# Optimization experiments

Measured on AMD Instinct MI355X. Metric: run time of the kernel, lower is better.

Reference implementation:

```python
import jax, jax.numpy as jnp
import numpy as np

N = 100000      # nodes
E = 1600000     # edges (avg degree 16)
IN = 512        # input feature dim
H, C = 8, 8     # conv1: 8 heads x 8 channels (hardcoded in module)
HID = H * C     # 64
OUT = 64        # output classes (conv2: 1 head, no concat)
NEG_SLOPE = 0.2 # PyG GATConv default leaky-relu slope


def setup_inputs() -> dict:
    key = jax.random.key(0)
    ks = jax.random.split(key, 10)
    x = jax.random.normal(ks[0], (N, IN), dtype=jnp.float32)
    edge_index = jax.random.randint(ks[1], (2, E), 0, N, dtype=jnp.int32)
    W1 = jax.random.normal(ks[2], (IN, HID), dtype=jnp.float32) / np.sqrt(IN).astype(np.float32)
    a_src1 = jax.random.normal(ks[3], (H, C), dtype=jnp.float32) * 0.1
    a_dst1 = jax.random.normal(ks[4], (H, C), dtype=jnp.float32) * 0.1
    b1 = jnp.zeros((HID,), dtype=jnp.float32)
    W2 = jax.random.normal(ks[5], (HID, OUT), dtype=jnp.float32) / np.sqrt(HID).astype(np.float32)
    a_src2 = jax.random.normal(ks[6], (1, OUT), dtype=jnp.float32) * 0.1
    a_dst2 = jax.random.normal(ks[7], (1, OUT), dtype=jnp.float32) * 0.1
    b2 = jnp.zeros((OUT,), dtype=jnp.float32)
    return {"x": x, "edge_index": edge_index, "W1": W1, "a_src1": a_src1,
            "a_dst1": a_dst1, "b1": b1, "W2": W2, "a_src2": a_src2,
            "a_dst2": a_dst2, "b2": b2}


def _gat_attend(h, src, dst, a_s, a_d, n_nodes):
    """h: [N,H,C]; src/dst: [E]; a_s/a_d: [H,C] -> aggregated [N,H,C]."""
    # per-node half-scores (PyG decomposition of a^T [Wx_i || Wx_j])
    sc_s = jnp.sum(h * a_s, axis=-1)                       # [N,H]
    sc_d = jnp.sum(h * a_d, axis=-1)                       # [N,H]
    logits = jax.nn.leaky_relu(sc_s[src] + sc_d[dst], NEG_SLOPE)  # [E,H]
    # segment softmax over edges grouped by destination node
    mx = jax.ops.segment_max(logits, dst, num_segments=n_nodes)   # [N,H]
    ex = jnp.exp(logits - mx[dst])                          # [E,H]
    denom = jax.ops.segment_sum(ex, dst, num_segments=n_nodes)    # [N,H]
    alpha = ex / (denom[dst] + 1e-16)                       # [E,H]
    msg = h[src] * alpha[:, :, None]                        # [E,H,C]
    return jax.ops.segment_sum(msg, dst, num_segments=n_nodes)    # [N,H,C]


def reference(x, edge_index, W1, a_src1, a_dst1, b1, W2, a_src2, a_dst2, b2):
    n = x.shape[0]
    loop = jnp.arange(n, dtype=edge_index.dtype)
    src = jnp.concatenate([edge_index[0], loop])            # self-loops (PyG default)
    dst = jnp.concatenate([edge_index[1], loop])
    # conv1: 8 heads, concat
    h1 = (x @ W1).reshape(n, H, C)
    o1 = _gat_attend(h1, src, dst, a_src1, a_dst1, n).reshape(n, HID) + b1
    x2 = jax.nn.elu(o1)
    # conv2: 1 head, no concat
    h2 = (x2 @ W2).reshape(n, 1, OUT)
    o2 = _gat_attend(h2, src, dst, a_src2, a_dst2, n)[:, 0] + b2
    return jax.nn.log_softmax(o2, axis=1)
```

## Files before the change

### kernel.cpp

```cpp
#include <hip/hip_runtime.h>
#include <cstdint>
#include <cstddef>

#define LEAKY 0.2f
#define NEG_INF -3.402823466e38f
static const int CHUNK = 2048;

typedef __attribute__((ext_vector_type(8))) short short8;
typedef __attribute__((ext_vector_type(4))) float floatx4;

__device__ __forceinline__ unsigned short f2bf(float f) {
    unsigned u = __float_as_uint(f);
    u += 0x7fffu + ((u >> 16) & 1u);
    return (unsigned short)(u >> 16);
}
__device__ __forceinline__ float bf2f(unsigned short u) {
    return __uint_as_float(((unsigned)u) << 16);
}
__device__ __forceinline__ float bflo(unsigned u) { return __uint_as_float(u << 16); }
__device__ __forceinline__ float bfhi(unsigned u) { return __uint_as_float(u & 0xffff0000u); }

__global__ __launch_bounds__(256) void k_misc(const float* __restrict__ W1, unsigned short* __restrict__ W1t,
                                              int* __restrict__ deg, int Nn) {
    int i = blockIdx.x * 256 + threadIdx.x;
    if (i < 64 * 512) {
        int n = i >> 9, k = i & 511;
        W1t[i] = f2bf(W1[k * 64 + n]);
    }
    if (i < Nn) deg[i] = 1;
}

__global__ __launch_bounds__(256) void k_mega1(const float* __restrict__ A, const unsigned short* __restrict__ W1t,
                                               unsigned short* __restrict__ C,
                                               const float* __restrict__ as1, const float* __restrict__ ad1,
                                               float* __restrict__ scs, float* __restrict__ scd, int M,
                                               const int* __restrict__ ei, int* __restrict__ deg, int E, int G1) {
    __shared__ __align__(16) unsigned short As[128][40];
    __shared__ __align__(16) unsigned short Bs[64][40];

    if ((int)blockIdx.x >= G1) {
        int cb = blockIdx.x - G1;
        int part = cb & 7;
        int Nn = M;
        int lo = (int)((long long)Nn * part >> 3);
        int hi = (int)((long long)Nn * (part + 1) >> 3);
        int nthr = (1024 >> 3) * 256;
        int tid = (cb >> 3) * 256 + threadIdx.x;
        for (int e = tid; e < E; e += nthr) {
            int d = ei[E + e];
            if (d >= lo && d < hi) atomicAdd(&deg[d], 1);
        }
        return;
    }

    int t = threadIdx.x;
    int w = t >> 6, l = t & 63;
    int quad = l >> 4, lm = l & 15;
    int row0 = blockIdx.x * 128;

    floatx4 acc[2][4] = {};

    for (int k0 = 0; k0 < 512; k0 += 32) {
#pragma unroll
        for (int j = 0; j < 4; ++j) {
            int f = t + 256 * j;
            int r = f >> 3, c4 = f & 7;
            int rg = row0 + r; if (rg >= M) rg = M - 1;
            float4 v = *(const float4*)(A + (size_t)rg * 512 + k0 + c4 * 4);
            ushort4 b; b.x = f2bf(v.x); b.y = f2bf(v.y); b.z = f2bf(v.z); b.w = f2bf(v.w);
            *(ushort4*)&As[r][c4 * 4] = b;
        }
        {
            int n = t >> 2, seg = t & 3;
            *(uint4*)&Bs[n][seg * 8] = *(const uint4*)(W1t + (size_t)n * 512 + k0 + seg * 8);
        }
        __syncthreads();

        short8 af[2], bfm[4];
#pragma unroll
        for (int tm = 0; tm < 2; ++tm) {
            int m = w * 32 + tm * 16 + lm;
            af[tm] = *(const short8*)&As[m][quad * 8];
        }
#pragma unroll
        for (int tn = 0; tn < 4; ++tn) {
            int n = tn * 16 + lm;
            bfm[tn] = *(const short8*)&Bs[n][quad * 8];
        }
#pragma unroll
        for (int tm = 0; tm < 2; ++tm)
#pragma unroll
            for (int tn = 0; tn < 4; ++tn)
                acc[tm][tn] = __builtin_amdgcn_mfma_f32_16x16x32_bf16(af[tm], bfm[tn], acc[tm][tn], 0, 0, 0);
        __syncthreads();
    }

    float as_l[4], ad_l[4];
#pragma unroll
    for (int tn = 0; tn < 4; ++tn) { as_l[tn] = as1[tn * 16 + lm]; ad_l[tn] = ad1[tn * 16 + lm]; }
    int hbase = (l >> 3) & 1;

#pragma unroll
    for (int tm = 0; tm < 2; ++tm) {
#pragma unroll
        for (int r = 0; r < 4; ++r) {
            int row = row0 + w * 32 + tm * 16 + quad * 4 + r;
            if (row < M) {
#pragma unroll
                for (int tn = 0; tn < 4; ++tn)
                    C[(size_t)row * 64 + tn * 16 + lm] = f2bf(acc[tm][tn][r]);
                float ps[4], pd[4];
#pragma unroll
                for (int tn = 0; tn < 4; ++tn) {
                    ps[tn] = acc[tm][tn][r] * as_l[tn];
                    pd[tn] = acc[tm][tn][r] * ad_l[tn];
                }
#pragma unroll
                for (int o = 1; o < 8; o <<= 1) {
#pragma unroll
                    for (int tn = 0; tn < 4; ++tn) {
                        ps[tn] += __shfl_xor(ps[tn], o);
                        pd[tn] += __shfl_xor(pd[tn], o);
                    }
                }
                if ((l & 7) == 0) {
#pragma unroll
                    for (int tn = 0; tn < 4; ++tn) {
                        scs[(size_t)row * 8 + tn * 2 + hbase] = ps[tn];
                        scd[(size_t)row * 8 + tn * 2 + hbase] = pd[tn];
                    }
                }
            }
        }
    }
}

__global__ __launch_bounds__(256) void k_scan1(const int* __restrict__ deg, int* __restrict__ bsum, int Nn) {
    __shared__ int sm[256];
    int b = blockIdx.x, t = threadIdx.x;
    int s = 0;
    int i0 = b * CHUNK + t * 8;
#pragma unroll
    for (int j = 0; j < 8; ++j) { int i = i0 + j; if (i < Nn) s += deg[i]; }
    sm[t] = s;
    __syncthreads();
    for (int o = 128; o; o >>= 1) { if (t < o) sm[t] += sm[t + o]; __syncthreads(); }
    if (t == 0) bsum[b] = sm[0];
}

__global__ __launch_bounds__(256) void k_scan3(const int* __restrict__ deg, const int* __restrict__ bsum,
                                               int* __restrict__ indptr, int* __restrict__ cursor,
                                               int Nn, int B) {
    __shared__ int wsum[4];
    int b = blockIdx.x, t = threadIdx.x, lane = t & 63, w = t >> 6;

    int vb = (lane < B) ? bsum[lane] : 0;
    int incb = vb;
#pragma unroll
    for (int o = 1; o < 64; o <<= 1) { int u = __shfl_up(incb, o); if (lane >= o) incb += u; }
    int bpre_b = __shfl(incb - vb, b);

    int i0 = b * CHUNK + t * 8;
    int d[8]; int s = 0;
#pragma unroll
    for (int j = 0; j < 8; ++j) { int i = i0 + j; d[j] = (i < Nn) ? deg[i] : 0; s += d[j]; }
    int inc = s;
#pragma unroll
    for (int o = 1; o < 64; o <<= 1) { int u = __shfl_up(inc, o); if (lane >= o) inc += u; }
    if (lane == 63) wsum[w] = inc;
    __syncthreads();
    int wofs = 0;
    for (int k = 0; k < w; ++k) wofs += wsum[k];
    int base = bpre_b + wofs + (inc - s);
    int run = 0;
#pragma unroll
    for (int j = 0; j < 8; ++j) {
        int i = i0 + j;
        if (i < Nn) {
            int v = base + run;
            indptr[i] = v; cursor[i] = v;
            run += d[j];
            if (i == Nn - 1) indptr[Nn] = v + d[j];
        }
    }
}

__global__ __launch_bounds__(256) void k_fill_p(const int* __restrict__ ei, int* __restrict__ cursor,
                                                int* __restrict__ csr, int E, int Nn) {
    int part = blockIdx.x & 7;
    int lo = (int)((long long)Nn * part >> 3);
    int hi = (int)((long long)Nn * (part + 1) >> 3);
    int nthr = (gridDim.x >> 3) * 256;
    int tid = (blockIdx.x >> 3) * 256 + threadIdx.x;
    int tot = E + Nn;
    for (int idx = tid; idx < tot; idx += nthr) {
        int d = (idx < E) ? ei[E + idx] : idx - E;
        if (d >= lo && d < hi) {
            int s = (idx < E) ? ei[idx] : idx - E;
            int slot = atomicAdd(&cursor[d], 1);
            csr[slot] = s;
        }
    }
}

template <int KB>
__global__ __launch_bounds__(256) void gemm_n64(const float* __restrict__ A, const float* __restrict__ B,
                                                unsigned short* __restrict__ C,
                                                const float* __restrict__ as2, const float* __restrict__ ad2,
                                                float* __restrict__ sc2s, float* __restrict__ sc2d,
                                                int M, int K) {
    __shared__ float As[KB][68];
    __shared__ float Bs[KB][68];
    int tid = threadIdx.x;
    int row0 = blockIdx.x * 64;
    int tx = tid & 15, ty = tid >> 4;
    float acc[4][4] = {};
    for (int k0 = 0; k0 < K; k0 += KB) {
#pragma unroll
        for (int j = 0; j < (64 * KB) / (256 * 4); ++j) {
            int f = tid + 256 * j;
            int r = f / (KB / 4);
            int c4 = f % (KB / 4);
            int rg = row0 + r; if (rg >= M) rg = M - 1;
            float4 v = *(const float4*)(A + (size_t)rg * K + k0 + c4 * 4);
            As[c4 * 4 + 0][r] = v.x; As[c4 * 4 + 1][r] = v.y;
            As[c4 * 4 + 2][r] = v.z; As[c4 * 4 + 3][r] = v.w;
        }
#pragma unroll
        for (int j = 0; j < (KB * 64) / (256 * 4); ++j) {
            int f = tid + 256 * j;
            int kk = f / 16, c4 = f % 16;
            *(float4*)&Bs[kk][c4 * 4] = *(const float4*)(B + (size_t)(k0 + kk) * 64 + c4 * 4);
        }
        __syncthreads();
#pragma unroll
        for (int kk = 0; kk < KB; ++kk) {
            float4 a = *(const float4*)&As[kk][ty * 4];
            float4 b = *(const float4*)&Bs[kk][tx * 4];
            float av[4] = {a.x, a.y, a.z, a.w};
            float bv[4] = {b.x, b.y, b.z, b.w};
#pragma unroll
            for (int i = 0; i < 4; ++i)
#pragma unroll
                for (int j = 0; j < 4; ++j) acc[i][j] += av[i] * bv[j];
        }
        __syncthreads();
    }
    float as_l[4], ad_l[4];
#pragma unroll
    for (int j = 0; j < 4; ++j) { as_l[j] = as2[tx * 4 + j]; ad_l[j] = ad2[tx * 4 + j]; }
#pragma unroll
    for (int i = 0; i < 4; ++i) {
        int rg = row0 + ty * 4 + i;
        if (rg < M) {
            ushort4 b; b.x = f2bf(acc[i][0]); b.y = f2bf(acc[i][1]);
            b.z = f2bf(acc[i][2]); b.w = f2bf(acc[i][3]);
            *(ushort4*)(C + (size_t)rg * 64 + tx * 4) = b;
            float ps = acc[i][0] * as_l[0] + acc[i][1] * as_l[1] + acc[i][2] * as_l[2] + acc[i][3] * as_l[3];
            float pd = acc[i][0] * ad_l[0] + acc[i][1] * ad_l[1] + acc[i][2] * ad_l[2] + acc[i][3] * ad_l[3];
#pragma unroll
            for (int o = 1; o < 16; o <<= 1) { ps += __shfl_xor(ps, o); pd += __shfl_xor(pd, o); }
            if (tx == 0) { sc2s[rg] = ps; sc2d[rg] = pd; }
        }
    }
}

__global__ __launch_bounds__(256) void k_agg1(const unsigned short* __restrict__ h1, const float* __restrict__ scs,
                                              const float* __restrict__ scd, const int* __restrict__ indptr,
                                              const int* __restrict__ csr, const float* __restrict__ b1,
                                              float* __restrict__ x2, int Nn) {
    int node = (blockIdx.x * 256 + threadIdx.x) >> 6;
    int l = threadIdx.x & 63;
    if (node >= Nn) return;
    int h8 = l & 7, grp = l >> 3;
    int start = indptr[node], end = indptr[node + 1];
    float sd = scd[node * 8 + h8];

    float dsum = 0.f;
    float acc8[8] = {};
    for (int base = start; base < end; base += 64) {
        int e = base + l;
        int s64 = csr[e < end ? e : start];
        int cnt = min(64, end - base);
        int nb = (cnt + 7) >> 3;
#pragma unroll
        for (int b = 0; b < 8; ++b) {
            if (b < nb) {
                int slot = base + b * 8 + grp;
                int sb = __shfl(s64, b * 8 + grp);
                float v = scs[sb * 8 + h8] + sd;
                v = v > 0.f ? v : LEAKY * v;
                float ex = (slot < end) ? __expf(v) : 0.f;
                dsum += ex;
                uint4 q = *(const uint4*)(h1 + (size_t)sb * 64 + h8 * 8);
                acc8[0] += ex * bflo(q.x); acc8[1] += ex * bfhi(q.x);
                acc8[2] += ex * bflo(q.y); acc8[3] += ex * bfhi(q.y);
                acc8[4] += ex * bflo(q.z); acc8[5] += ex * bfhi(q.z);
                acc8[6] += ex * bflo(q.w); acc8[7] += ex * bfhi(q.w);
            }
        }
    }
#pragma unroll
    for (int o = 8; o < 64; o <<= 1) {
        dsum += __shfl_xor(dsum, o);
#pragma unroll
        for (int k = 0; k < 8; ++k) acc8[k] += __shfl_xor(acc8[k], o);
    }
    if (grp == 0) {
        float inv = 1.f / (dsum + 1e-16f);
        float4 ba = *((const float4*)b1 + h8 * 2);
        float4 bb = *((const float4*)b1 + h8 * 2 + 1);
        float o0 = acc8[0] * inv + ba.x, o1 = acc8[1] * inv + ba.y;
        float o2 = acc8[2] * inv + ba.z, o3 = acc8[3] * inv + ba.w;
        float o4 = acc8[4] * inv + bb.x, o5 = acc8[5] * inv + bb.y;
        float o6 = acc8[6] * inv + bb.z, o7 = acc8[7] * inv + bb.w;
        o0 = o0 > 0.f ? o0 : expm1f(o0); o1 = o1 > 0.f ? o1 : expm1f(o1);
        o2 = o2 > 0.f ? o2 : expm1f(o2); o3 = o3 > 0.f ? o3 : expm1f(o3);
        o4 = o4 > 0.f ? o4 : expm1f(o4); o5 = o5 > 0.f ? o5 : expm1f(o5);
        o6 = o6 > 0.f ? o6 : expm1f(o6); o7 = o7 > 0.f ? o7 : expm1f(o7);
        float* dst = x2 + (size_t)node * 64 + h8 * 8;
        *(float4*)dst = make_float4(o0, o1, o2, o3);
        *(float4*)(dst + 4) = make_float4(o4, o5, o6, o7);
    }
}

__global__ __launch_bounds__(256) void k_agg2(const unsigned short* __restrict__ h2, const float* __restrict__ scs,
                                              const float* __restrict__ scd, const int* __restrict__ indptr,
                                              const int* __restrict__ csr, const float* __restrict__ b2,
                                              float* __restrict__ out, int Nn) {
    int node = (blockIdx.x * 256 + threadIdx.x) >> 6;
    int l = threadIdx.x & 63;
    if (node >= Nn) return;
    int g = l >> 3, c8 = l & 7;
    int start = indptr[node], end = indptr[node + 1];
    float sd = scd[node];

    float dsum = 0.f;
    float acc8[8] = {};
    for (int base = start; base < end; base += 64) {
        int e = base + l;
        int s64 = csr[e < end ? e : start];
        float v = scs[s64] + sd;
        v = v > 0.f ? v : LEAKY * v;
        float ex = (e < end) ? __expf(v) : 0.f;
        dsum += ex;
        int cnt = min(64, end - base);
        int nb = (cnt + 7) >> 3;
#pragma unroll 2
        for (int b = 0; b < nb; ++b) {
            float exv = __shfl(ex, b * 8 + g);
            int sb = __shfl(s64, b * 8 + g);
            uint4 q = *(const uint4*)(h2 + (size_t)sb * 64 + c8 * 8);
            acc8[0] += exv * bflo(q.x); acc8[1] += exv * bfhi(q.x);
            acc8[2] += exv * bflo(q.y); acc8[3] += exv * bfhi(q.y);
            acc8[4] += exv * bflo(q.z); acc8[5] += exv * bfhi(q.z);
            acc8[6] += exv * bflo(q.w); acc8[7] += exv * bfhi(q.w);
        }
    }
#pragma unroll
    for (int o = 32; o; o >>= 1) dsum += __shfl_xor(dsum, o);
#pragma unroll
    for (int o = 8; o < 64; o <<= 1)
#pragma unroll
        for (int k = 0; k < 8; ++k) acc8[k] += __shfl_xor(acc8[k], o);

    float inv = 1.f / (dsum + 1e-16f);
    float4 ba = *((const float4*)b2 + c8 * 2);
    float4 bb = *((const float4*)b2 + c8 * 2 + 1);
    float ov[8];
    ov[0] = acc8[0] * inv + ba.x; ov[1] = acc8[1] * inv + ba.y;
    ov[2] = acc8[2] * inv + ba.z; ov[3] = acc8[3] * inv + ba.w;
    ov[4] = acc8[4] * inv + bb.x; ov[5] = acc8[5] * inv + bb.y;
    ov[6] = acc8[6] * inv + bb.z; ov[7] = acc8[7] * inv + bb.w;

    float m2 = ov[0];
#pragma unroll
    for (int k = 1; k < 8; ++k) m2 = fmaxf(m2, ov[k]);
#pragma unroll
    for (int o = 1; o < 8; o <<= 1) m2 = fmaxf(m2, __shfl_xor(m2, o));
    float se = 0.f;
#pragma unroll
    for (int k = 0; k < 8; ++k) se += __expf(ov[k] - m2);
#pragma unroll
    for (int o = 1; o < 8; o <<= 1) se += __shfl_xor(se, o);
    float ls = m2 + __logf(se);
    if (g == 0) {
        float* dst = out + (size_t)node * 64 + c8 * 8;
        *(float4*)dst = make_float4(ov[0] - ls, ov[1] - ls, ov[2] - ls, ov[3] - ls);
        *(float4*)(dst + 4) = make_float4(ov[4] - ls, ov[5] - ls, ov[6] - ls, ov[7] - ls);
    }
}

extern "C" void kernel_launch(void* const* d_in, const int* in_sizes, int n_in,
                              void* d_out, int out_size, void* d_ws, size_t ws_size,
                              hipStream_t stream) {
    (void)n_in; (void)out_size; (void)ws_size;
    const float* x   = (const float*)d_in[0];
    const int*   ei  = (const int*)d_in[1];
    const float* W1  = (const float*)d_in[2];
    const float* as1 = (const float*)d_in[3];
    const float* ad1 = (const float*)d_in[4];
    const float* b1  = (const float*)d_in[5];
    const float* W2  = (const float*)d_in[6];
    const float* as2 = (const float*)d_in[7];
    const float* ad2 = (const float*)d_in[8];
    const float* b2  = (const float*)d_in[9];
    float* out = (float*)d_out;

    const int N = in_sizes[0] / 512;
    const int E = in_sizes[1] / 2;

    char* p = (char*)d_ws;
    auto alloc = [&](size_t bytes) -> char* {
        char* r = p; p += (bytes + 255) & ~(size_t)255; return r;
    };
    unsigned short* h1bf = (unsigned short*)alloc((size_t)N * 64 * 2);
    float* x2    = (float*)alloc((size_t)N * 64 * 4);
    unsigned short* h2bf = h1bf;
    float* sc1s  = (float*)alloc((size_t)N * 8 * 4);
    float* sc1d  = (float*)alloc((size_t)N * 8 * 4);
    float* sc2s  = (float*)alloc((size_t)N * 4);
    float* sc2d  = (float*)alloc((size_t)N * 4);
    int*   deg   = (int*)alloc((size_t)N * 4);
    int*   cursor= (int*)alloc((size_t)N * 4);
    int*   indptr= (int*)alloc((size_t)(N + 1) * 4);
    int*   csr   = (int*)alloc((size_t)(E + N) * 4);
    int*   bsum  = (int*)alloc(64 * 4);
    unsigned short* W1t = (unsigned short*)alloc(64 * 512 * 2);

    const int B = (N + CHUNK - 1) / CHUNK;
    const int G1 = (N + 127) / 128;

    const int miscGrid = (((64 * 512) > N ? (64 * 512) : N) + 255) / 256;
    k_misc<<<miscGrid, 256, 0, stream>>>(W1, W1t, deg, N);

    k_mega1<<<G1 + 1024, 256, 0, stream>>>(x, W1t, h1bf, as1, ad1, sc1s, sc1d, N,
                                           ei, deg, E, G1);

    k_scan1 <<<B, 256, 0, stream>>>(deg, bsum, N);
    k_scan3 <<<B, 256, 0, stream>>>(deg, bsum, indptr, cursor, N, B);
    k_fill_p<<<1024, 256, 0, stream>>>(ei, cursor, csr, E, N);

    k_agg1<<<(N + 3) / 4, 256, 0, stream>>>(h1bf, sc1s, sc1d, indptr, csr, b1, x2, N);

    gemm_n64<64><<<(N + 63) / 64, 256, 0, stream>>>(x2, W2, h2bf, as2, ad2, sc2s, sc2d, N, 64);

    k_agg2<<<(N + 3) / 4, 256, 0, stream>>>(h2bf, sc2s, sc2d, indptr, csr, b2, out, N);
}
```

Before: 592.1 us.

## Double-buffer LDS tiles and prefetch next K-slice in GEMM kernel

The x@W1 GEMM in k_mega1 now uses two LDS buffers. Global loads for the next K-slice are issued into registers before the MFMAs on the current slice, then converted and stored to the other buffer, so one barrier per iteration replaces two. The aim is to hide global memory latency behind MFMA work, at the cost of doubled shared memory and more registers held live.

```diff
diff --git a/kernel.cpp b/kernel.cpp
--- a/kernel.cpp
+++ b/kernel.cpp
@@ -35,8 +35,8 @@
                                                const float* __restrict__ as1, const float* __restrict__ ad1,
                                                float* __restrict__ scs, float* __restrict__ scd, int M,
                                                const int* __restrict__ ei, int* __restrict__ deg, int E, int G1) {
-    __shared__ __align__(16) unsigned short As[128][40];
-    __shared__ __align__(16) unsigned short Bs[64][40];
+    __shared__ __align__(16) unsigned short As[2][128][40];
+    __shared__ __align__(16) unsigned short Bs[2][64][40];
 
     if ((int)blockIdx.x >= G1) {
         int cb = blockIdx.x - G1;
@@ -58,40 +58,69 @@
     int quad = l >> 4, lm = l & 15;
     int row0 = blockIdx.x * 128;
 
+    const float* aptr[4];
+#pragma unroll
+    for (int j = 0; j < 4; ++j) {
+        int f = t + 256 * j;
+        int r = f >> 3, c4 = f & 7;
+        int rg = row0 + r; if (rg >= M) rg = M - 1;
+        aptr[j] = A + (size_t)rg * 512 + c4 * 4;
+    }
+    int bn = t >> 2, bseg = t & 3;
+    const unsigned short* bptr = W1t + (size_t)bn * 512 + bseg * 8;
+    int sr = t >> 3, sc4 = t & 7;
+
     floatx4 acc[2][4] = {};
-
-    for (int k0 = 0; k0 < 512; k0 += 32) {
-#pragma unroll
-        for (int j = 0; j < 4; ++j) {
-            int f = t + 256 * j;
-            int r = f >> 3, c4 = f & 7;
-            int rg = row0 + r; if (rg >= M) rg = M - 1;
-            float4 v = *(const float4*)(A + (size_t)rg * 512 + k0 + c4 * 4);
-            ushort4 b; b.x = f2bf(v.x); b.y = f2bf(v.y); b.z = f2bf(v.z); b.w = f2bf(v.w);
-            *(ushort4*)&As[r][c4 * 4] = b;
-        }
-        {
-            int n = t >> 2, seg = t & 3;
-            *(uint4*)&Bs[n][seg * 8] = *(const uint4*)(W1t + (size_t)n * 512 + k0 + seg * 8);
-        }
-        __syncthreads();
+    float4 va[4];
+    uint4 vb;
+
+#pragma unroll
+    for (int j = 0; j < 4; ++j) va[j] = *(const float4*)(aptr[j] + 0);
+    vb = *(const uint4*)(bptr + 0);
+#pragma unroll
+    for (int j = 0; j < 4; ++j) {
+        ushort4 b; b.x = f2bf(va[j].x); b.y = f2bf(va[j].y); b.z = f2bf(va[j].z); b.w = f2bf(va[j].w);
+        *(ushort4*)&As[0][sr + 32 * j][sc4 * 4] = b;
+    }
+    *(uint4*)&Bs[0][bn][bseg * 8] = vb;
+    __syncthreads();
+
+#pragma unroll
+    for (int kt = 0; kt < 16; ++kt) {
+        int cur = kt & 1;
+        if (kt < 15) {
+            int k0 = (kt + 1) * 32;
+#pragma unroll
+            for (int j = 0; j < 4; ++j) va[j] = *(const float4*)(aptr[j] + k0);
+            vb = *(const uint4*)(bptr + k0);
+        }
 
         short8 af[2], bfm[4];
 #pragma unroll
         for (int tm = 0; tm < 2; ++tm) {
             int m = w * 32 + tm * 16 + lm;
-            af[tm] = *(const short8*)&As[m][quad * 8];
+            af[tm] = *(const short8*)&As[cur][m][quad * 8];
         }
 #pragma unroll
         for (int tn = 0; tn < 4; ++tn) {
             int n = tn * 16 + lm;
-            bfm[tn] = *(const short8*)&Bs[n][quad * 8];
+            bfm[tn] = *(const short8*)&Bs[cur][n][quad * 8];
         }
 #pragma unroll
         for (int tm = 0; tm < 2; ++tm)
 #pragma unroll
             for (int tn = 0; tn < 4; ++tn)
                 acc[tm][tn] = __builtin_amdgcn_mfma_f32_16x16x32_bf16(af[tm], bfm[tn], acc[tm][tn], 0, 0, 0);
+
+        if (kt < 15) {
+            int nxt = cur ^ 1;
+#pragma unroll
+            for (int j = 0; j < 4; ++j) {
+                ushort4 b; b.x = f2bf(va[j].x); b.y = f2bf(va[j].y); b.z = f2bf(va[j].z); b.w = f2bf(va[j].w);
+                *(ushort4*)&As[nxt][sr + 32 * j][sc4 * 4] = b;
+            }
+            *(uint4*)&Bs[nxt][bn][bseg * 8] = vb;
+        }
         __syncthreads();
     }
 
```

Result: no change. 583.5 us (-1.4%).
